# Performance work log

Measured on AMD Instinct MI355X. Metric: run time of the kernel, lower is better.

## Reference

```python
import jax, jax.numpy as jnp
import numpy as np

B, N, D, H = 2, 2048, 1024, 16
DH = D // H  # 64


def setup_inputs() -> dict:
    key = jax.random.key(0)
    k1, k2, k3, k4, k5 = jax.random.split(key, 5)
    x = jax.random.normal(k1, (B, N, D), dtype=jnp.float32)
    # per-head kqv Linear weights, stacked: [H, D, 3*DH] (acts as x @ W)
    W_kqv = jax.random.normal(k2, (H, D, 3 * DH), dtype=jnp.float32) * 0.02
    b_kqv = jax.random.normal(k3, (H, 3 * DH), dtype=jnp.float32) * 0.02
    W_proj = jax.random.normal(k4, (D, D), dtype=jnp.float32) * 0.02
    b_proj = jax.random.normal(k5, (D,), dtype=jnp.float32) * 0.02
    return {"x": x, "W_kqv": W_kqv, "b_kqv": b_kqv, "W_proj": W_proj, "b_proj": b_proj}


def reference(x, W_kqv, b_kqv, W_proj, b_proj):
    # per-head projections, all heads batched: [B, H, N, 3*DH]
    kqv = jnp.einsum('bnd,hde->bhne', x, W_kqv) + b_kqv[None, :, None, :]
    # original chunk order is k, q, v
    k, q, v = jnp.split(kqv, 3, axis=-1)  # each [B, H, N, DH]
    # scores: A = q @ k^T / sqrt(DH)  -> [B, H, N, N]
    A = jnp.einsum('bhnd,bhmd->bhnm', q, k) / jnp.sqrt(jnp.asarray(DH, x.dtype))
    causal = jnp.tril(jnp.ones((N, N), dtype=bool))
    A = jnp.where(causal[None, None, :, :], A, -jnp.inf)
    attn = jax.nn.softmax(A, axis=-1)
    sa = jnp.einsum('bhnm,bhmd->bhnd', attn, v)          # [B, H, N, DH]
    sa = sa.transpose(0, 2, 1, 3).reshape(B, N, D)        # concat heads
    out = sa @ W_proj.T + b_proj                          # output projection
    return out
```

## Files before the change

kernel.cpp:

```cpp
#include <hip/hip_runtime.h>
#include <hip/hip_bf16.h>
#include <cstdint>
#include <cstddef>

#define B_  2
#define N_  2048
#define D_  1024
#define H_  16
#define DH_ 64
#define E3_ 192

typedef __attribute__((ext_vector_type(8))) short short8;
typedef __attribute__((ext_vector_type(8))) unsigned short ushort8v;
typedef __attribute__((ext_vector_type(4))) float floatx4;

static __device__ __forceinline__ unsigned short f2bf(float f) {
  union { float f; unsigned u; } c; c.f = f;
  unsigned r = c.u + 0x7fffu + ((c.u >> 16) & 1u);
  return (unsigned short)(r >> 16);
}

#define MFMA(a,b,c) __builtin_amdgcn_mfma_f32_16x16x32_bf16((a),(b),(c),0,0,0)

#define GL_LDS16(g, l) __builtin_amdgcn_global_load_lds( \
    (const __attribute__((address_space(1))) void*)(g),  \
    (__attribute__((address_space(3))) void*)(l), 16, 0, 0)

__global__ __launch_bounds__(256) void k_prep(const float* __restrict__ x,
                                              const float* __restrict__ Wkqv,
                                              const float* __restrict__ Wproj,
                                              unsigned short* __restrict__ Xb,
                                              unsigned short* __restrict__ Wt,
                                              unsigned short* __restrict__ Wpb) {
  __shared__ float tile[64][65];
  int bx = blockIdx.x, t = threadIdx.x;
  if (bx < 2048 || bx >= 2816) {
    const float* in = (bx < 2048) ? x : Wproj;
    unsigned short* out = (bx < 2048) ? Xb : Wpb;
    int i = ((bx < 2048) ? bx : bx - 2816) * 256 + t;
    const float4* p = (const float4*)in + (size_t)i * 2;
    float4 a = p[0], b = p[1];
    ushort8v o;
    o[0]=f2bf(a.x); o[1]=f2bf(a.y); o[2]=f2bf(a.z); o[3]=f2bf(a.w);
    o[4]=f2bf(b.x); o[5]=f2bf(b.y); o[6]=f2bf(b.z); o[7]=f2bf(b.w);
    *((ushort8v*)out + i) = o;
    return;
  }
  int idx = bx - 2048;
  int d0 = (idx & 15) * 64, rem = idx >> 4;
  int cat = rem % 3, h = rem / 3, e0 = cat * 64;
  const float* Wp = Wkqv + (size_t)h * D_ * E3_;
  int dr = t >> 2, ec = (t & 3) * 16;
#pragma unroll
  for (int j = 0; j < 16; j += 4) {
    float4 wv = *(const float4*)&Wp[(size_t)(d0 + dr) * E3_ + e0 + ec + j];
    tile[dr][ec + j + 0] = wv.x; tile[dr][ec + j + 1] = wv.y;
    tile[dr][ec + j + 2] = wv.z; tile[dr][ec + j + 3] = wv.w;
  }
  __syncthreads();
  int er = t >> 2, dc = (t & 3) * 16;
  ushort8v o0, o1;
#pragma unroll
  for (int j = 0; j < 8; j++) o0[j] = f2bf(tile[dc + j][er]);
#pragma unroll
  for (int j = 0; j < 8; j++) o1[j] = f2bf(tile[dc + 8 + j][er]);
  size_t o = ((size_t)(cat * 1024 + h * 64 + er)) * D_ + d0 + dc;
  *(ushort8v*)&Wt[o]     = o0;
  *(ushort8v*)&Wt[o + 8] = o1;
}

__global__ __launch_bounds__(256) void k_qkv(const unsigned short* __restrict__ Xb,
                                             const unsigned short* __restrict__ Wt,
                                             const float* __restrict__ bkqv,
                                             unsigned short* __restrict__ Qb,
                                             unsigned short* __restrict__ Kb,
                                             unsigned short* __restrict__ Vt) {
  __shared__ unsigned short Alds[2][128 * 32];
  __shared__ unsigned short Blds[2][128 * 32];
  int t = threadIdx.x;
  int m0 = blockIdx.x * 128, c0 = blockIdx.y * 128;
  int wave = t >> 6, lane = t & 63, quad = lane >> 4, l16 = lane & 15;
  int wm = (wave >> 1) * 64, wn = (wave & 1) * 64;
  floatx4 acc[4][4];
#pragma unroll
  for (int i = 0; i < 4; i++)
#pragma unroll
    for (int j = 0; j < 4; j++) acc[i][j] = (floatx4){0.f, 0.f, 0.f, 0.f};

  int swz = ((lane & 3) ^ ((lane >> 3) & 3)) * 8;
  const unsigned short* gA = Xb + (size_t)(m0 + wave * 32 + (lane >> 2)) * D_ + swz;
  const unsigned short* gB = Wt + (size_t)(c0 + wave * 32 + (lane >> 2)) * D_ + swz;
  int lofs = (wave * 32) * 32;
  int xr = ((l16 >> 1) & 3) * 8;

  GL_LDS16(gA,            &Alds[0][lofs]);
  GL_LDS16(gA + 16 * D_,  &Alds[0][lofs + 16 * 32]);
  GL_LDS16(gB,            &Blds[0][lofs]);
  GL_LDS16(gB + 16 * D_,  &Blds[0][lofs + 16 * 32]);

  for (int i = 0; i < 32; i++) {
    int buf = i & 1;
    __syncthreads();
    if (i + 1 < 32) {
      int k0 = (i + 1) * 32;
      GL_LDS16(gA + k0,            &Alds[buf ^ 1][lofs]);
      GL_LDS16(gA + k0 + 16 * D_,  &Alds[buf ^ 1][lofs + 16 * 32]);
      GL_LDS16(gB + k0,            &Blds[buf ^ 1][lofs]);
      GL_LDS16(gB + k0 + 16 * D_,  &Blds[buf ^ 1][lofs + 16 * 32]);
    }
    short8 a[4], b[4];
#pragma unroll
    for (int mi = 0; mi < 4; mi++) a[mi] = *(const short8*)&Alds[buf][(wm + mi * 16 + l16) * 32 + ((quad * 8) ^ xr)];
#pragma unroll
    for (int ni = 0; ni < 4; ni++) b[ni] = *(const short8*)&Blds[buf][(wn + ni * 16 + l16) * 32 + ((quad * 8) ^ xr)];
#pragma unroll
    for (int mi = 0; mi < 4; mi++)
#pragma unroll
      for (int ni = 0; ni < 4; ni++) acc[mi][ni] = MFMA(a[mi], b[ni], acc[mi][ni]);
  }

  __syncthreads();
  unsigned short* scratch = ((wave < 2) ? &Alds[0][0] : &Blds[0][0]) + (wave & 1) * 4096;
  int cat = c0 >> 10;
  float scale = (cat == 1) ? 0.125f : 1.0f;
#pragma unroll
  for (int mi = 0; mi < 4; mi++)
#pragma unroll
    for (int ni = 0; ni < 4; ni++) {
      int lc = ni * 16 + l16;
      int colp = c0 + wn + lc;
      int h = (colp >> 6) & 15, e = colp & 63;
      float bias = bkqv[h * E3_ + cat * 64 + e];
#pragma unroll
      for (int r = 0; r < 4; r++) {
        unsigned short val = f2bf((acc[mi][ni][r] + bias) * scale);
        int lr = mi * 16 + quad * 4 + r;
        if (cat < 2)
          scratch[lr * 64 + (((lc >> 3) ^ (lr & 7)) * 8) + (lc & 7)] = val;
        else
          scratch[lc * 64 + (((lr >> 3) ^ (lc & 7)) * 8) + (lr & 7)] = val;
      }
    }
  __asm__ volatile("s_waitcnt lgkmcnt(0)" ::: "memory");
  int l8 = lane & 7, lh = lane >> 3;
  if (cat < 2) {
    unsigned short* dst = (cat == 0) ? Kb : Qb;
#pragma unroll
    for (int j = 0; j < 8; j++) {
      int lr = j * 8 + lh;
      short8 vv = *(const short8*)&scratch[lr * 64 + ((l8 ^ lh) * 8)];
      int grow = m0 + wm + lr;
      int b = grow >> 11, n0 = grow & (N_ - 1);
      int colp = c0 + wn + l8 * 8;
      int h = (colp >> 6) & 15, e0 = colp & 63;
      *(short8*)&dst[((size_t)(b * H_ + h) * N_ + n0) * DH_ + e0] = vv;
    }
  } else {
#pragma unroll
    for (int j = 0; j < 8; j++) {
      int le = j * 8 + lh;
      short8 vv = *(const short8*)&scratch[le * 64 + ((l8 ^ lh) * 8)];
      int colp = c0 + wn + le;
      int h = (colp >> 6) & 15, e = colp & 63;
      int grow = m0 + wm;
      int b = grow >> 11, n0 = (grow & (N_ - 1)) + l8 * 8;
      *(short8*)&Vt[((size_t)(b * H_ + h) * DH_ + e) * N_ + n0] = vv;
    }
  }
}

__global__ __launch_bounds__(256) void k_flash(const unsigned short* __restrict__ Qb,
                                               const unsigned short* __restrict__ Kb,
                                               const unsigned short* __restrict__ Vt,
                                               unsigned short* __restrict__ sab) {
  int bh = blockIdx.x;
  int yr = blockIdx.y, g = yr >> 3, o = yr & 7;
  int qb = (g == 0) ? o : (g == 1) ? 31 - o : (g == 2) ? 8 + o : 23 - o;
  int q0b = qb * 64;
  int wave = threadIdx.x >> 6;
  int lane = threadIdx.x & 63, quad = lane >> 4, l16 = lane & 15;
  const unsigned short* Qp = Qb + (size_t)bh * N_ * DH_;
  const unsigned short* Kp = Kb + (size_t)bh * N_ * DH_;
  const unsigned short* Vp = Vt + (size_t)bh * DH_ * N_;
  __shared__ unsigned short Klds[2][2 * 64 * 32];
  __shared__ unsigned short Vlds[2][2 * 64 * 32];
  __shared__ unsigned short Plds[4][16 * 64];
  unsigned short* P = Plds[wave];

  int q0w = q0b + wave * 16;
  short8 qf0 = *(const short8*)&Qp[(q0w + l16) * DH_ + quad * 8];
  short8 qf1 = *(const short8*)&Qp[(q0w + l16) * DH_ + 32 + quad * 8];

  int swz = ((lane & 3) ^ ((lane >> 3) & 3)) * 8;
  const unsigned short* gK = Kp + (size_t)(wave * 16 + (lane >> 2)) * DH_ + swz;
  const unsigned short* gV = Vp + (size_t)(wave * 16 + (lane >> 2)) * N_ + swz;
  int lofs = (wave * 16) * 32;
  int xr = ((l16 >> 1) & 3) * 8;
  int pxr = l16 & 7;

  floatx4 O[4];
  float lr[4];
#pragma unroll
  for (int r = 0; r < 4; r++) { O[r] = (floatx4){0.f, 0.f, 0.f, 0.f}; lr[r] = 0.f; }

  int nt = (q0b >> 6) + 1;
  GL_LDS16(gK,      &Klds[0][lofs]);
  GL_LDS16(gK + 32, &Klds[0][lofs + 64 * 32]);
  GL_LDS16(gV,      &Vlds[0][lofs]);
  GL_LDS16(gV + 32, &Vlds[0][lofs + 64 * 32]);

  for (int i = 0; i < nt; i++) {
    int buf = i & 1;
    __syncthreads();
    if (i + 1 < nt) {
      int kvn = (i + 1) << 6;
      GL_LDS16(gK + (size_t)kvn * DH_,      &Klds[buf ^ 1][lofs]);
      GL_LDS16(gK + (size_t)kvn * DH_ + 32, &Klds[buf ^ 1][lofs + 64 * 32]);
      GL_LDS16(gV + kvn,                    &Vlds[buf ^ 1][lofs]);
      GL_LDS16(gV + kvn + 32,               &Vlds[buf ^ 1][lofs + 64 * 32]);
    }
    short8 kf[4][2], vf[4][2];
#pragma unroll
    for (int c = 0; c < 4; c++) {
      kf[c][0] = *(const short8*)&Klds[buf][(c * 16 + l16) * 32 + ((quad * 8) ^ xr)];
      kf[c][1] = *(const short8*)&Klds[buf][(64 + c * 16 + l16) * 32 + ((quad * 8) ^ xr)];
      vf[c][0] = *(const short8*)&Vlds[buf][(c * 16 + l16) * 32 + ((quad * 8) ^ xr)];
      vf[c][1] = *(const short8*)&Vlds[buf][(64 + c * 16 + l16) * 32 + ((quad * 8) ^ xr)];
    }
    floatx4 s[4];
#pragma unroll
    for (int c = 0; c < 4; c++) {
      s[c] = (floatx4){0.f, 0.f, 0.f, 0.f};
      s[c] = MFMA(qf0, kf[c][0], s[c]);
      s[c] = MFMA(qf1, kf[c][1], s[c]);
    }
    if (i == nt - 1) {
#pragma unroll
      for (int c = 0; c < 4; c++)
#pragma unroll
        for (int r = 0; r < 4; r++) {
          int row = wave * 16 + quad * 4 + r;
          if (c * 16 + l16 > row) s[c][r] = -1e30f;
        }
    }
#pragma unroll
    for (int c = 0; c < 4; c++)
#pragma unroll
      for (int r = 0; r < 4; r++)
        s[c][r] = __builtin_amdgcn_exp2f(s[c][r] * 1.44269504f);
#pragma unroll
    for (int r = 0; r < 4; r++)
      lr[r] += (s[0][r] + s[1][r]) + (s[2][r] + s[3][r]);
#pragma unroll
    for (int c = 0; c < 4; c++) {
      int ch = c * 2 + (l16 >> 3);
#pragma unroll
      for (int r = 0; r < 4; r++) {
        int row = quad * 4 + r;
        P[row * 64 + ((ch ^ (row & 7)) * 8) + (l16 & 7)] = f2bf(s[c][r]);
      }
    }
    __asm__ volatile("s_waitcnt lgkmcnt(0)" ::: "memory");
    short8 pa0 = *(const short8*)&P[l16 * 64 + ((quad ^ pxr) * 8)];
    short8 pa1 = *(const short8*)&P[l16 * 64 + (((quad + 4) ^ pxr) * 8)];
    __asm__ volatile("" ::: "memory");
#pragma unroll
    for (int dt = 0; dt < 4; dt++) {
      O[dt] = MFMA(pa0, vf[dt][0], O[dt]);
      O[dt] = MFMA(pa1, vf[dt][1], O[dt]);
    }
  }
#pragma unroll
  for (int m = 1; m < 16; m <<= 1)
#pragma unroll
    for (int r = 0; r < 4; r++) lr[r] += __shfl_xor(lr[r], m);

  int b = bh >> 4, h = bh & 15;
#pragma unroll
  for (int r = 0; r < 4; r++) {
    float inv = 1.0f / lr[r];
    size_t base = ((size_t)b * N_ + q0w + quad * 4 + r) * D_ + h * DH_;
#pragma unroll
    for (int dt = 0; dt < 4; dt++) sab[base + dt * 16 + l16] = f2bf(O[dt][r] * inv);
  }
}

__global__ __launch_bounds__(256) void k_proj(const unsigned short* __restrict__ sab,
                                              const unsigned short* __restrict__ Wpb,
                                              const float* __restrict__ bproj,
                                              float* __restrict__ out) {
  __shared__ unsigned short Alds[2][2][64 * 32];
  __shared__ unsigned short Blds[2][2][64 * 32];
  int t = threadIdx.x;
  int m0 = blockIdx.x * 64, c0 = blockIdx.y * 64;
  int wave = t >> 6, lane = t & 63, quad = lane >> 4, l16 = lane & 15;
  int wm = (wave >> 1) * 32, wn = (wave & 1) * 32;
  floatx4 acc[2][2];
#pragma unroll
  for (int i = 0; i < 2; i++) { acc[i][0] = (floatx4){0,0,0,0}; acc[i][1] = (floatx4){0,0,0,0}; }

  int swz = ((lane & 3) ^ ((lane >> 3) & 3)) * 8;
  const unsigned short* gA = sab + (size_t)(m0 + wave * 16 + (lane >> 2)) * D_ + swz;
  const unsigned short* gB = Wpb + (size_t)(c0 + wave * 16 + (lane >> 2)) * D_ + swz;
  int lofs = (wave * 16) * 32;
  int xr = ((l16 >> 1) & 3) * 8;

  GL_LDS16(gA,      &Alds[0][0][lofs]);
  GL_LDS16(gA + 32, &Alds[0][1][lofs]);
  GL_LDS16(gB,      &Blds[0][0][lofs]);
  GL_LDS16(gB + 32, &Blds[0][1][lofs]);

  for (int i = 0; i < 16; i++) {
    int buf = i & 1;
    __syncthreads();
    if (i + 1 < 16) {
      int k0 = (i + 1) * 64;
      GL_LDS16(gA + k0,      &Alds[buf ^ 1][0][lofs]);
      GL_LDS16(gA + k0 + 32, &Alds[buf ^ 1][1][lofs]);
      GL_LDS16(gB + k0,      &Blds[buf ^ 1][0][lofs]);
      GL_LDS16(gB + k0 + 32, &Blds[buf ^ 1][1][lofs]);
    }
#pragma unroll
    for (int kk = 0; kk < 2; kk++) {
      short8 a[2], b[2];
#pragma unroll
      for (int mi = 0; mi < 2; mi++) a[mi] = *(const short8*)&Alds[buf][kk][(wm + mi * 16 + l16) * 32 + ((quad * 8) ^ xr)];
#pragma unroll
      for (int ni = 0; ni < 2; ni++) b[ni] = *(const short8*)&Blds[buf][kk][(wn + ni * 16 + l16) * 32 + ((quad * 8) ^ xr)];
#pragma unroll
      for (int mi = 0; mi < 2; mi++)
#pragma unroll
        for (int ni = 0; ni < 2; ni++) acc[mi][ni] = MFMA(a[mi], b[ni], acc[mi][ni]);
    }
  }
#pragma unroll
  for (int mi = 0; mi < 2; mi++)
#pragma unroll
    for (int ni = 0; ni < 2; ni++) {
      int col = c0 + wn + ni * 16 + l16;
      int grow = m0 + wm + mi * 16 + quad * 4;
      float bias = bproj[col];
#pragma unroll
      for (int r = 0; r < 4; r++)
        out[(size_t)(grow + r) * D_ + col] = acc[mi][ni][r] + bias;
    }
}

extern "C" void kernel_launch(void* const* d_in, const int* in_sizes, int n_in,
                              void* d_out, int out_size, void* d_ws, size_t ws_size,
                              hipStream_t stream) {
  const float* x     = (const float*)d_in[0];
  const float* Wkqv  = (const float*)d_in[1];
  const float* bkqv  = (const float*)d_in[2];
  const float* Wproj = (const float*)d_in[3];
  const float* bproj = (const float*)d_in[4];
  float* out = (float*)d_out;

  char* w = (char*)d_ws;
  unsigned short* Xb  = (unsigned short*)(w);
  unsigned short* Wt  = (unsigned short*)(w + (8u  << 20));
  unsigned short* Wpb = (unsigned short*)(w + (14u << 20));
  unsigned short* Qb  = (unsigned short*)(w + (16u << 20));
  unsigned short* Kb  = (unsigned short*)(w + (24u << 20));
  unsigned short* Vt  = (unsigned short*)(w + (32u << 20));
  unsigned short* sa  = (unsigned short*)(w + (40u << 20));

  k_prep<<<2048 + 768 + 512, 256, 0, stream>>>(x, Wkqv, Wproj, Xb, Wt, Wpb);
  k_qkv<<<dim3(B_ * N_ / 128, 3072 / 128), 256, 0, stream>>>(Xb, Wt, bkqv, Qb, Kb, Vt);
  k_flash<<<dim3(B_ * H_, N_ / 64), 256, 0, stream>>>(Qb, Kb, Vt, sa);
  k_proj<<<dim3(B_ * N_ / 64, D_ / 64), 256, 0, stream>>>(sa, Wpb, bproj, out);
}
```

Before: 186.0 us.

## Rewrite QKV GEMM as 256x256 tile, 8-wave pipelined kernel

The QKV projection GEMM moves from 128x128 tiles with 4 waves and K-step 32 to 256x256 tiles with 8 waves and K-step 64, using a single 128 KB LDS buffer. The main loop is split into four phases with barriers, setprio and sched_barrier, so that LDS reads and global-to-LDS prefetches overlap with MFMA work. The epilogue is simplified because each wave tile now maps to exactly one head. The grid becomes 16x12=192 blocks, which may underfill the 256 CUs, and the large LDS footprint limits occupancy.

```diff
diff --git a/kernel.cpp b/kernel.cpp
--- a/kernel.cpp
+++ b/kernel.cpp
@@ -69,104 +69,186 @@
   *(ushort8v*)&Wt[o + 8] = o1;
 }
 
-__global__ __launch_bounds__(256) void k_qkv(const unsigned short* __restrict__ Xb,
-                                             const unsigned short* __restrict__ Wt,
-                                             const float* __restrict__ bkqv,
-                                             unsigned short* __restrict__ Qb,
-                                             unsigned short* __restrict__ Kb,
-                                             unsigned short* __restrict__ Vt) {
-  __shared__ unsigned short Alds[2][128 * 32];
-  __shared__ unsigned short Blds[2][128 * 32];
-  int t = threadIdx.x;
-  int m0 = blockIdx.x * 128, c0 = blockIdx.y * 128;
-  int wave = t >> 6, lane = t & 63, quad = lane >> 4, l16 = lane & 15;
-  int wm = (wave >> 1) * 64, wn = (wave & 1) * 64;
-  floatx4 acc[4][4];
-#pragma unroll
-  for (int i = 0; i < 4; i++)
+__global__ __launch_bounds__(512, 2) void k_qkv(const unsigned short* __restrict__ Xb,
+                                                const unsigned short* __restrict__ Wt,
+                                                const float* __restrict__ bkqv,
+                                                unsigned short* __restrict__ Qb,
+                                                unsigned short* __restrict__ Kb,
+                                                unsigned short* __restrict__ Vt) {
+  __shared__ unsigned short LDSf[65536];
+  const int t = threadIdx.x;
+  const int wid = t >> 6, lane = t & 63, quad = lane >> 4, l16 = lane & 15;
+  const int wr = wid >> 2, wc = wid & 3;
+  const int m0 = blockIdx.x * 256, c0 = blockIdx.y * 256;
+
+  floatx4 acc[8][4];
+#pragma unroll
+  for (int i = 0; i < 8; i++)
 #pragma unroll
     for (int j = 0; j < 4; j++) acc[i][j] = (floatx4){0.f, 0.f, 0.f, 0.f};
 
-  int swz = ((lane & 3) ^ ((lane >> 3) & 3)) * 8;
-  const unsigned short* gA = Xb + (size_t)(m0 + wave * 32 + (lane >> 2)) * D_ + swz;
-  const unsigned short* gB = Wt + (size_t)(c0 + wave * 32 + (lane >> 2)) * D_ + swz;
-  int lofs = (wave * 32) * 32;
-  int xr = ((l16 >> 1) & 3) * 8;
-
-  GL_LDS16(gA,            &Alds[0][lofs]);
-  GL_LDS16(gA + 16 * D_,  &Alds[0][lofs + 16 * 32]);
-  GL_LDS16(gB,            &Blds[0][lofs]);
-  GL_LDS16(gB + 16 * D_,  &Blds[0][lofs + 16 * 32]);
-
-  for (int i = 0; i < 32; i++) {
-    int buf = i & 1;
-    __syncthreads();
-    if (i + 1 < 32) {
-      int k0 = (i + 1) * 32;
-      GL_LDS16(gA + k0,            &Alds[buf ^ 1][lofs]);
-      GL_LDS16(gA + k0 + 16 * D_,  &Alds[buf ^ 1][lofs + 16 * 32]);
-      GL_LDS16(gB + k0,            &Blds[buf ^ 1][lofs]);
-      GL_LDS16(gB + k0 + 16 * D_,  &Blds[buf ^ 1][lofs + 16 * 32]);
-    }
-    short8 a[4], b[4];
-#pragma unroll
-    for (int mi = 0; mi < 4; mi++) a[mi] = *(const short8*)&Alds[buf][(wm + mi * 16 + l16) * 32 + ((quad * 8) ^ xr)];
-#pragma unroll
-    for (int ni = 0; ni < 4; ni++) b[ni] = *(const short8*)&Blds[buf][(wn + ni * 16 + l16) * 32 + ((quad * 8) ^ xr)];
+  const int slr = t >> 3;
+  const int sco = ((t & 7) ^ (slr & 7)) * 8;
+  const unsigned short* gA0 = Xb + (size_t)(m0 +   0 + slr) * D_ + sco;
+  const unsigned short* gA1 = Xb + (size_t)(m0 +  64 + slr) * D_ + sco;
+  const unsigned short* gA2 = Xb + (size_t)(m0 + 128 + slr) * D_ + sco;
+  const unsigned short* gA3 = Xb + (size_t)(m0 + 192 + slr) * D_ + sco;
+  const unsigned short* gB0 = Wt + (size_t)(c0 +   0 + slr) * D_ + sco;
+  const unsigned short* gB1 = Wt + (size_t)(c0 +  64 + slr) * D_ + sco;
+  const unsigned short* gB2 = Wt + (size_t)(c0 + 128 + slr) * D_ + sco;
+  const unsigned short* gB3 = Wt + (size_t)(c0 + 192 + slr) * D_ + sco;
+#define SA(gp, q, s, bb) GL_LDS16((gp) + (s) * 64, &LDSf[(bb) * 16384 + (q) * 4096 + t * 8])
+#define SB(gp, q, s, bb) GL_LDS16((gp) + (s) * 64, &LDSf[32768 + (bb) * 16384 + (q) * 4096 + t * 8])
+
+  const int aoff0 = ((quad)     ^ (l16 & 7)) * 8;
+  const int aoff1 = ((4 + quad) ^ (l16 & 7)) * 8;
+  const unsigned short* Abase = &LDSf[(wr * 128 + l16) * 64];
+  const unsigned short* Bbase = &LDSf[32768 + (wc * 64 + l16) * 64];
+
+  SA(gA0, 0, 0, 0); SA(gA1, 1, 0, 0); SA(gA2, 2, 0, 0); SA(gA3, 3, 0, 0);
+  SB(gB0, 0, 0, 0); SB(gB1, 1, 0, 0); SB(gB2, 2, 0, 0); SB(gB3, 3, 0, 0);
+  SA(gA0, 0, 1, 1); SA(gA2, 2, 1, 1);
+  asm volatile("s_waitcnt vmcnt(2)" ::: "memory");
+  __builtin_amdgcn_s_barrier();
+
+  for (int s = 0; s < 16; s++) {
+    const int buf = s & 1, nbuf = buf ^ 1;
+    const int so = buf * 16384;
+    short8 a[4][2], b[4][2];
+#pragma unroll
+    for (int mi = 0; mi < 4; mi++) {
+      a[mi][0] = *(const short8*)&Abase[so + mi * 1024 + aoff0];
+      a[mi][1] = *(const short8*)&Abase[so + mi * 1024 + aoff1];
+    }
+#pragma unroll
+    for (int ni = 0; ni < 2; ni++) {
+      b[ni][0] = *(const short8*)&Bbase[so + ni * 1024 + aoff0];
+      b[ni][1] = *(const short8*)&Bbase[so + ni * 1024 + aoff1];
+    }
+    if (s < 15) {
+      SA(gA1, 1, s + 1, nbuf); SA(gA3, 3, s + 1, nbuf);
+      SB(gB0, 0, s + 1, nbuf); SB(gB1, 1, s + 1, nbuf);
+      SB(gB2, 2, s + 1, nbuf); SB(gB3, 3, s + 1, nbuf);
+    }
+    __builtin_amdgcn_s_barrier();
+    asm volatile("s_waitcnt lgkmcnt(0)" ::: "memory");
+    __builtin_amdgcn_sched_barrier(0);
+    __builtin_amdgcn_s_setprio(1);
 #pragma unroll
     for (int mi = 0; mi < 4; mi++)
 #pragma unroll
-      for (int ni = 0; ni < 4; ni++) acc[mi][ni] = MFMA(a[mi], b[ni], acc[mi][ni]);
+      for (int ni = 0; ni < 2; ni++) {
+        acc[mi][ni] = MFMA(a[mi][0], b[ni][0], acc[mi][ni]);
+        acc[mi][ni] = MFMA(a[mi][1], b[ni][1], acc[mi][ni]);
+      }
+    __builtin_amdgcn_s_setprio(0);
+    __builtin_amdgcn_s_barrier();
+#pragma unroll
+    for (int ni = 2; ni < 4; ni++) {
+      b[ni][0] = *(const short8*)&Bbase[so + ni * 1024 + aoff0];
+      b[ni][1] = *(const short8*)&Bbase[so + ni * 1024 + aoff1];
+    }
+    __builtin_amdgcn_s_barrier();
+    asm volatile("s_waitcnt lgkmcnt(0)" ::: "memory");
+    __builtin_amdgcn_sched_barrier(0);
+    __builtin_amdgcn_s_setprio(1);
+#pragma unroll
+    for (int mi = 0; mi < 4; mi++)
+#pragma unroll
+      for (int ni = 2; ni < 4; ni++) {
+        acc[mi][ni] = MFMA(a[mi][0], b[ni][0], acc[mi][ni]);
+        acc[mi][ni] = MFMA(a[mi][1], b[ni][1], acc[mi][ni]);
+      }
+    __builtin_amdgcn_s_setprio(0);
+    __builtin_amdgcn_s_barrier();
+#pragma unroll
+    for (int mi = 0; mi < 4; mi++) {
+      a[mi][0] = *(const short8*)&Abase[so + (mi + 4) * 1024 + aoff0];
+      a[mi][1] = *(const short8*)&Abase[so + (mi + 4) * 1024 + aoff1];
+    }
+    if (s < 14) { SA(gA0, 0, s + 2, buf); SA(gA2, 2, s + 2, buf); }
+    __builtin_amdgcn_s_barrier();
+    asm volatile("s_waitcnt lgkmcnt(0)" ::: "memory");
+    __builtin_amdgcn_sched_barrier(0);
+    __builtin_amdgcn_s_setprio(1);
+#pragma unroll
+    for (int mi = 0; mi < 4; mi++)
+#pragma unroll
+      for (int ni = 0; ni < 2; ni++) {
+        acc[mi + 4][ni] = MFMA(a[mi][0], b[ni][0], acc[mi + 4][ni]);
+        acc[mi + 4][ni] = MFMA(a[mi][1], b[ni][1], acc[mi + 4][ni]);
+      }
+    __builtin_amdgcn_s_setprio(0);
+    __builtin_amdgcn_s_barrier();
+    __builtin_amdgcn_s_setprio(1);
+#pragma unroll
+    for (int mi = 0; mi < 4; mi++)
+#pragma unroll
+      for (int ni = 2; ni < 4; ni++) {
+        acc[mi + 4][ni] = MFMA(a[mi][0], b[ni][0], acc[mi + 4][ni]);
+        acc[mi + 4][ni] = MFMA(a[mi][1], b[ni][1], acc[mi + 4][ni]);
+      }
+    __builtin_amdgcn_s_setprio(0);
+    if (s < 14) { asm volatile("s_waitcnt vmcnt(2)" ::: "memory"); }
+    else        { asm volatile("s_waitcnt vmcnt(0)" ::: "memory"); }
+    __builtin_amdgcn_s_barrier();
   }
 
   __syncthreads();
-  unsigned short* scratch = ((wave < 2) ? &Alds[0][0] : &Blds[0][0]) + (wave & 1) * 4096;
-  int cat = c0 >> 10;
-  float scale = (cat == 1) ? 0.125f : 1.0f;
-#pragma unroll
-  for (int mi = 0; mi < 4; mi++)
-#pragma unroll
-    for (int ni = 0; ni < 4; ni++) {
-      int lc = ni * 16 + l16;
-      int colp = c0 + wn + lc;
-      int h = (colp >> 6) & 15, e = colp & 63;
-      float bias = bkqv[h * E3_ + cat * 64 + e];
-#pragma unroll
-      for (int r = 0; r < 4; r++) {
-        unsigned short val = f2bf((acc[mi][ni][r] + bias) * scale);
-        int lr = mi * 16 + quad * 4 + r;
-        if (cat < 2)
-          scratch[lr * 64 + (((lc >> 3) ^ (lr & 7)) * 8) + (lc & 7)] = val;
-        else
-          scratch[lc * 64 + (((lr >> 3) ^ (lc & 7)) * 8) + (lr & 7)] = val;
-      }
-    }
-  __asm__ volatile("s_waitcnt lgkmcnt(0)" ::: "memory");
-  int l8 = lane & 7, lh = lane >> 3;
+  unsigned short* scr = &LDSf[wid * 8192];
+  const int cat = c0 >> 10;
+  const int h   = ((c0 + wc * 64) >> 6) & 15;
+  const int bb  = (m0 + wr * 128) >> 11;
+  const int n0b = (m0 + wr * 128) & (N_ - 1);
+  const int l8 = lane & 7, lh = lane >> 3;
   if (cat < 2) {
+    const float scale = (cat == 1) ? 0.125f : 1.0f;
+    float bias[4];
+#pragma unroll
+    for (int ni = 0; ni < 4; ni++) bias[ni] = bkqv[h * E3_ + cat * 64 + ni * 16 + l16];
+#pragma unroll
+    for (int mi = 0; mi < 8; mi++)
+#pragma unroll
+      for (int ni = 0; ni < 4; ni++)
+#pragma unroll
+        for (int r = 0; r < 4; r++) {
+          int rl = mi * 16 + quad * 4 + r, cl = ni * 16 + l16;
+          scr[rl * 64 + ((((cl >> 3) ^ rl) & 7) * 8) + (cl & 7)] =
+              f2bf((acc[mi][ni][r] + bias[ni]) * scale);
+        }
+    asm volatile("s_waitcnt lgkmcnt(0)" ::: "memory");
     unsigned short* dst = (cat == 0) ? Kb : Qb;
 #pragma unroll
-    for (int j = 0; j < 8; j++) {
-      int lr = j * 8 + lh;
-      short8 vv = *(const short8*)&scratch[lr * 64 + ((l8 ^ lh) * 8)];
-      int grow = m0 + wm + lr;
-      int b = grow >> 11, n0 = grow & (N_ - 1);
-      int colp = c0 + wn + l8 * 8;
-      int h = (colp >> 6) & 15, e0 = colp & 63;
-      *(short8*)&dst[((size_t)(b * H_ + h) * N_ + n0) * DH_ + e0] = vv;
+    for (int j = 0; j < 16; j++) {
+      int rl = j * 8 + lh;
+      short8 vv = *(const short8*)&scr[rl * 64 + ((l8 ^ lh) * 8)];
+      *(short8*)&dst[((size_t)(bb * H_ + h) * N_ + n0b + rl) * DH_ + l8 * 8] = vv;
     }
   } else {
-#pragma unroll
-    for (int j = 0; j < 8; j++) {
-      int le = j * 8 + lh;
-      short8 vv = *(const short8*)&scratch[le * 64 + ((l8 ^ lh) * 8)];
-      int colp = c0 + wn + le;
-      int h = (colp >> 6) & 15, e = colp & 63;
-      int grow = m0 + wm;
-      int b = grow >> 11, n0 = (grow & (N_ - 1)) + l8 * 8;
-      *(short8*)&Vt[((size_t)(b * H_ + h) * DH_ + e) * N_ + n0] = vv;
-    }
-  }
+    float bias[4];
+#pragma unroll
+    for (int ni = 0; ni < 4; ni++) bias[ni] = bkqv[h * E3_ + 128 + ni * 16 + l16];
+#pragma unroll
+    for (int mi = 0; mi < 8; mi++)
+#pragma unroll
+      for (int ni = 0; ni < 4; ni++)
+#pragma unroll
+        for (int r = 0; r < 4; r++) {
+          int nl = mi * 16 + quad * 4 + r, e = ni * 16 + l16;
+          scr[e * 128 + ((((nl >> 3) ^ e) & 15) * 8) + (nl & 7)] =
+              f2bf(acc[mi][ni][r] + bias[ni]);
+        }
+    asm volatile("s_waitcnt lgkmcnt(0)" ::: "memory");
+#pragma unroll
+    for (int j = 0; j < 16; j++) {
+      int e = (j & 7) * 8 + lh;
+      int nc = l8 + (j >> 3) * 8;
+      short8 vv = *(const short8*)&scr[e * 128 + (((nc ^ e) & 15) * 8)];
+      *(short8*)&Vt[((size_t)(bb * H_ + h) * DH_ + e) * N_ + n0b + nc * 8] = vv;
+    }
+  }
+#undef SA
+#undef SB
 }
 
 __global__ __launch_bounds__(256) void k_flash(const unsigned short* __restrict__ Qb,
@@ -366,7 +448,7 @@
   unsigned short* sa  = (unsigned short*)(w + (40u << 20));
 
   k_prep<<<2048 + 768 + 512, 256, 0, stream>>>(x, Wkqv, Wproj, Xb, Wt, Wpb);
-  k_qkv<<<dim3(B_ * N_ / 128, 3072 / 128), 256, 0, stream>>>(Xb, Wt, bkqv, Qb, Kb, Vt);
+  k_qkv<<<dim3(B_ * N_ / 256, 3072 / 256), 512, 0, stream>>>(Xb, Wt, bkqv, Qb, Kb, Vt);
   k_flash<<<dim3(B_ * H_, N_ / 64), 256, 0, stream>>>(Qb, Kb, Vt, sa);
   k_proj<<<dim3(B_ * N_ / 64, D_ / 64), 256, 0, stream>>>(sa, Wpb, bproj, out);
 }
```

New measurement: 179.1 us. 3.7% less time.
